# Optimization experiments

Hardware: AMD Instinct MI355X
Metric: run time of the kernel (lower is better)

Reference implementation:

```python
import jax, jax.numpy as jnp
import numpy as np
import math

HEAD_DIM = 128
DEPTH = 12
LAMBDA_INIT = 0.8 - 0.6 * math.exp(-0.3 * DEPTH)
EPS = 1e-5
SCALE = 1.0 / math.sqrt(HEAD_DIM / 2)


def setup_inputs() -> dict:
    key = jax.random.key(0)
    ks = jax.random.split(key, 8)
    b, t, d = 2, 4096, 2048
    return {
        "x": jax.random.normal(ks[0], (b, t, d), dtype=jnp.float32),
        "wq": jax.random.normal(ks[1], (d, HEAD_DIM), dtype=jnp.float32) * 0.02,
        "wk": jax.random.normal(ks[2], (d, HEAD_DIM), dtype=jnp.float32) * 0.02,
        "wv": jax.random.normal(ks[3], (d, HEAD_DIM), dtype=jnp.float32) * 0.02,
        "lambda_q1": jax.random.normal(ks[4], (HEAD_DIM // 2,), dtype=jnp.float32) * 0.1,
        "lambda_q2": jax.random.normal(ks[5], (HEAD_DIM // 2,), dtype=jnp.float32) * 0.1,
        "lambda_k1": jax.random.normal(ks[6], (HEAD_DIM // 2,), dtype=jnp.float32) * 0.1,
        "lambda_k2": jax.random.normal(ks[7], (HEAD_DIM // 2,), dtype=jnp.float32) * 0.1,
        "ln_weight": jnp.ones((HEAD_DIM,), dtype=jnp.float32),
    }


def reference(x, wq, wk, wv, lambda_q1, lambda_q2, lambda_k1, lambda_k2, ln_weight):
    b, t, d = x.shape
    q = x @ wq  # [b,t,hd]
    k = x @ wk
    v = x @ wv
    h = HEAD_DIM // 2
    q1, q2 = q[..., :h], q[..., h:]
    k1, k2 = k[..., :h], k[..., h:]
    # causal mask: True where attention is disallowed (strictly upper triangle)
    causal = jnp.triu(jnp.ones((t, t), dtype=bool), k=1)
    neg_inf = jnp.float32(-jnp.inf)

    def masked_softmax(qh, kh):
        scores = jnp.einsum('btd,bsd->bts', qh, kh) * SCALE
        scores = jnp.where(causal, neg_inf, scores)
        return jax.nn.softmax(scores, axis=-1)

    a1 = masked_softmax(q1, k1)
    a2 = masked_softmax(q2, k2)
    lmbda = (jnp.exp(jnp.sum(lambda_q1 * lambda_k1))
             - jnp.exp(jnp.sum(lambda_q2 * lambda_k2))
             + LAMBDA_INIT)
    diffattn = jnp.einsum('bts,bsd->btd', a1 - lmbda * a2, v)
    rms = jnp.sqrt(jnp.mean(diffattn * diffattn, axis=-1, keepdims=True) + EPS)
    out = (1.0 - LAMBDA_INIT) * (diffattn / rms * ln_weight)
    return out
```

## Files before the change

kernel.cpp:

```cpp
#include <hip/hip_runtime.h>
#include <stdint.h>

#define T_SEQ 4096
#define NB 2
#define D_MODEL 2048
#define HD 128

typedef __attribute__((ext_vector_type(4)))  float f32x4;
typedef __attribute__((ext_vector_type(16))) float f32x16;
typedef __attribute__((ext_vector_type(8)))  short bf16x8;
typedef __attribute__((ext_vector_type(4)))  unsigned u32x4;

#define LAMBDA_INIT 0.7836057665316244f
#define OUT_SCALE   0.21639423346837556f

__device__ __forceinline__ unsigned short f2bf(float f) {
  unsigned int u = __float_as_uint(f);
  u += 0x7FFFu + ((u >> 16) & 1u);
  return (unsigned short)(u >> 16);
}
__device__ __forceinline__ float bf2f(unsigned short h) {
  return __uint_as_float(((unsigned int)h) << 16);
}
__device__ __forceinline__ unsigned cvt_pk_bf16(float a, float b) {
  unsigned r;
  asm("v_cvt_pk_bf16_f32 %0, %1, %2" : "=v"(r) : "v"(a), "v"(b));
  return r;
}
__device__ __forceinline__ void gload16(const void* g, void* l) {
  __builtin_amdgcn_global_load_lds(
      (const __attribute__((address_space(1))) unsigned int*)g,
      (__attribute__((address_space(3))) unsigned int*)l, 16, 0, 0);
}

__global__ __launch_bounds__(256) void wtrans(
    const float* __restrict__ wq, const float* __restrict__ wk,
    const float* __restrict__ wv, unsigned short* __restrict__ wT)
{
  const int which = blockIdx.y;
  const int s = blockIdx.x;
  const float* w = (which == 0) ? wq : ((which == 1) ? wk : wv);
  const float scale = (which == 0) ? 0.125f : 1.0f;
  const int tid = threadIdx.x;
  #pragma unroll
  for (int j = 0; j < 4; ++j) {
    int cell = j * 256 + tid;
    int q = cell >> 7, n = cell & 127;
    int kb = s * 64 + q * 8;
    float v[8];
    #pragma unroll
    for (int e = 0; e < 8; ++e) v[e] = w[(size_t)(kb + e) * HD + n] * scale;
    u32x4 pk = { cvt_pk_bf16(v[0], v[1]), cvt_pk_bf16(v[2], v[3]),
                 cvt_pk_bf16(v[4], v[5]), cvt_pk_bf16(v[6], v[7]) };
    *reinterpret_cast<u32x4*>(&wT[(size_t)(which * 32 + s) * 8192 + (size_t)cell * 8]) = pk;
  }
}

__global__ __launch_bounds__(256, 2) void qkv_part(
    const float* __restrict__ x, const unsigned short* __restrict__ wT,
    float* __restrict__ P)
{
  __shared__ __align__(16) char lds[4][16384];
  const int tid = threadIdx.x, lane = tid & 63, wid = tid >> 6;
  const int bid = blockIdx.x;
  const int ks   = bid & 1;
  const int type = (bid >> 1) % 3;
  const int mt   = bid / 6;
  const int wm = wid >> 1, wn = wid & 1;
  const int fr = lane & 15, fq = lane >> 4;
  const int m0 = mt * 64;

  const float* xbase = x + (size_t)m0 * D_MODEL + ks * 1024;
  const unsigned short* wslab = wT + (size_t)type * 262144 + (size_t)(ks * 16) * 8192;

  f32x4 acc[2][4];
  #pragma unroll
  for (int i = 0; i < 2; ++i)
    #pragma unroll
    for (int j = 0; j < 4; ++j) acc[i][j] = (f32x4){0.f, 0.f, 0.f, 0.f};

#define DMA(t) do {                                                        \
    char* As_ = &lds[(t) & 3][0];                                          \
    char* Bs_ = &lds[(t) & 3][8192];                                       \
    const int k0_ = (t) * 32;                                              \
    _Pragma("unroll")                                                      \
    for (int j = 0; j < 2; ++j) {                                          \
      int c = (wid * 2 + j) * 64 + lane;                                   \
      int row = c >> 3, kcp = c & 7;                                       \
      gload16(xbase + (size_t)row * D_MODEL + k0_ + ((kcp ^ (row & 7)) << 2), \
              As_ + (wid * 2 + j) * 1024);                                 \
    }                                                                      \
    const unsigned short* bsrc_ = wslab + (size_t)(t) * 4096;              \
    _Pragma("unroll")                                                      \
    for (int j = 0; j < 2; ++j) {                                          \
      int cb = (wid * 2 + j) * 64;                                         \
      gload16(bsrc_ + (size_t)(cb + lane) * 8, Bs_ + cb * 16);             \
    }                                                                      \
  } while (0)

#define STEP(t, VMIMM) do {                                                \
    asm volatile("s_waitcnt vmcnt(" VMIMM ")" ::: "memory");               \
    __builtin_amdgcn_s_barrier();                                          \
    __builtin_amdgcn_sched_barrier(0);                                     \
    if ((t) + 3 < 32) DMA((t) + 3);                                        \
    __builtin_amdgcn_sched_barrier(0);                                     \
    const char* Ac_ = &lds[(t) & 3][0];                                    \
    const char* Bc_ = &lds[(t) & 3][8192];                                 \
    bf16x8 af_[2];                                                         \
    _Pragma("unroll")                                                      \
    for (int mi = 0; mi < 2; ++mi) {                                       \
      int row = wm * 32 + mi * 16 + fr;                                    \
      int p1 = (2 * fq) ^ (row & 7), p2 = (2 * fq + 1) ^ (row & 7);        \
      f32x4 lo = *reinterpret_cast<const f32x4*>(Ac_ + (row * 8 + p1) * 16); \
      f32x4 hi = *reinterpret_cast<const f32x4*>(Ac_ + (row * 8 + p2) * 16); \
      u32x4 pk = { cvt_pk_bf16(lo[0], lo[1]), cvt_pk_bf16(lo[2], lo[3]),   \
                   cvt_pk_bf16(hi[0], hi[1]), cvt_pk_bf16(hi[2], hi[3]) }; \
      af_[mi] = *reinterpret_cast<bf16x8*>(&pk);                           \
    }                                                                      \
    _Pragma("unroll")                                                      \
    for (int ni = 0; ni < 4; ++ni) {                                       \
      int n = wn * 64 + ni * 16 + fr;                                      \
      bf16x8 bf_ = *reinterpret_cast<const bf16x8*>(Bc_ + (fq * 128 + n) * 16); \
      acc[0][ni] = __builtin_amdgcn_mfma_f32_16x16x32_bf16(af_[0], bf_, acc[0][ni], 0, 0, 0); \
      acc[1][ni] = __builtin_amdgcn_mfma_f32_16x16x32_bf16(af_[1], bf_, acc[1][ni], 0, 0, 0); \
    }                                                                      \
  } while (0)

  DMA(0); DMA(1); DMA(2);
  #pragma unroll 1
  for (int t = 0; t < 30; ++t) STEP(t, "8");
  STEP(30, "4");
  STEP(31, "0");
#undef STEP
#undef DMA

  float* pp = P + ((size_t)(ks * 3 + type) * 8192 + m0) * 128;
  #pragma unroll
  for (int mi = 0; mi < 2; ++mi)
    #pragma unroll
    for (int ni = 0; ni < 4; ++ni)
      #pragma unroll
      for (int r = 0; r < 4; ++r)
        pp[(size_t)(wm * 32 + mi * 16 + fq * 4 + r) * 128 + wn * 64 + ni * 16 + fr]
            = acc[mi][ni][r];
}

__global__ __launch_bounds__(256) void qkv_merge(
    const float* __restrict__ P,
    unsigned short* __restrict__ qb, unsigned short* __restrict__ kS,
    unsigned short* __restrict__ vS)
{
  const int gid = blockIdx.x * 256 + threadIdx.x;
  const size_t e8 = (size_t)gid * 8;
  const int type = (int)(e8 >> 20);
  const int rem  = (int)(e8 & 1048575);
  const int m = rem >> 7, n0 = rem & 127;
  const float* p0 = P + (size_t)type * 1048576 + rem;
  const float* p1 = p0 + (size_t)3 * 1048576;
  f32x4 a0 = *reinterpret_cast<const f32x4*>(p0);
  f32x4 a1 = *reinterpret_cast<const f32x4*>(p0 + 4);
  f32x4 b0 = *reinterpret_cast<const f32x4*>(p1);
  f32x4 b1 = *reinterpret_cast<const f32x4*>(p1 + 4);
  float s[8];
  #pragma unroll
  for (int j = 0; j < 4; ++j) { s[j] = a0[j] + b0[j]; s[4 + j] = a1[j] + b1[j]; }
  u32x4 pk = { cvt_pk_bf16(s[0], s[1]), cvt_pk_bf16(s[2], s[3]),
               cvt_pk_bf16(s[4], s[5]), cvt_pk_bf16(s[6], s[7]) };

  const int bb = m >> 12, tt = m & 4095;
  const int kt = tt >> 5, kvl = tt & 31;
  if (type == 0) {
    *reinterpret_cast<u32x4*>(&qb[(size_t)m * HD + n0]) = pk;
  } else if (type == 1) {
    int g = n0 >> 6, hl = n0 & 63;
    int ksf = hl >> 4, r8 = (hl >> 3) & 1;
    size_t idx = ((((((size_t)bb * 128 + kt) * 2 + g) * 4) + ksf) << 9)
               + (size_t)(kvl + 32 * r8) * 8;
    *reinterpret_cast<u32x4*>(&kS[idx]) = pk;
  } else {
    int f = kvl >> 4, r8v = (kvl >> 3) & 1, e = kvl & 7;
    #pragma unroll
    for (int j = 0; j < 8; ++j) {
      int n = n0 + j;
      int vcb = n >> 5;
      size_t idx = (((((size_t)bb * 128 + kt) * 8) + vcb * 2 + f) << 9)
                 + (size_t)((n & 31) + 32 * r8v) * 8 + e;
      vS[idx] = f2bf(s[j]);
    }
  }
}

template<int LOG2S>
__global__ __launch_bounds__(256, 2) void diff_attn_part(
    const unsigned short* __restrict__ qb, const unsigned short* __restrict__ kS,
    const unsigned short* __restrict__ vS,
    unsigned short* __restrict__ po, float* __restrict__ pm, float* __restrict__ pl)
{
  constexpr int S = 1 << LOG2S;
  const int tid = threadIdx.x, lane = tid & 63, wid = tid >> 6;
  const int wave_id = blockIdx.x * 4 + wid;
  const int sp = wave_id & (S - 1);
  const int g  = (wave_id >> LOG2S) & 1;
  const int qt_raw = (wave_id >> (LOG2S + 1)) & 127;
  const int b  = wave_id >> (LOG2S + 8);
  const int qt = 127 - qt_raw;
  const int slot = (((b * 128 + qt) * 2 + g) << LOG2S) + sp;
  const int lq = lane & 31, lh = lane >> 5;
  const int q0 = qt * 32;
  const int n  = qt + 1;
  const int kt0 = (n * sp) >> LOG2S;
  const int kt1 = (n * (sp + 1)) >> LOG2S;

  bf16x8 qf[4];
  const unsigned short* qp = qb + ((size_t)b * T_SEQ + q0 + lq) * HD + g * 64 + lh * 8;
  #pragma unroll
  for (int ks = 0; ks < 4; ++ks) qf[ks] = *reinterpret_cast<const bf16x8*>(qp + ks * 16);

  f32x16 acc[4];
  #pragma unroll
  for (int v = 0; v < 4; ++v)
    #pragma unroll
    for (int r = 0; r < 16; ++r) acc[v][r] = 0.f;
  float mrun = -1e30f, lrun = 0.f;

  const unsigned short* kbase = kS + ((size_t)(b * 128) * 2 + g) * 4 * 512 + lane * 8;
  const unsigned short* vbase = vS + (size_t)(b * 128) * 8 * 512 + lane * 8;
  #define KFRAG(kt, ks) (kbase + ((size_t)(kt) * 8 + (ks)) * 512)
  #define VFRAG(kt, f)  (vbase + ((size_t)(kt) * 8 + (f)) * 512)

  bf16x8 kf[4];
  if (kt0 < kt1) {
    #pragma unroll
    for (int ks = 0; ks < 4; ++ks)
      kf[ks] = *reinterpret_cast<const bf16x8*>(KFRAG(kt0, ks));
  }

  for (int kt = kt0; kt < kt1; ++kt) {
    bf16x8 vfa[4], vfb[4];
    #pragma unroll
    for (int vcb = 0; vcb < 4; ++vcb) {
      vfa[vcb] = *reinterpret_cast<const bf16x8*>(VFRAG(kt, vcb * 2));
      vfb[vcb] = *reinterpret_cast<const bf16x8*>(VFRAG(kt, vcb * 2 + 1));
    }
    bf16x8 kfn[4];
    const bool more = (kt + 1 < kt1);
    if (more) {
      #pragma unroll
      for (int ks = 0; ks < 4; ++ks)
        kfn[ks] = *reinterpret_cast<const bf16x8*>(KFRAG(kt + 1, ks));
    }
    f32x16 sc;
    #pragma unroll
    for (int r = 0; r < 16; ++r) sc[r] = 0.f;
    #pragma unroll
    for (int ks = 0; ks < 4; ++ks)
      sc = __builtin_amdgcn_mfma_f32_32x32x16_bf16(kf[ks], qf[ks], sc, 0, 0, 0);

    float p[16];
    if (kt == n - 1) {
      #pragma unroll
      for (int r = 0; r < 16; ++r) {
        int rloc = (r & 3) + 8 * (r >> 2) + 4 * lh;
        p[r] = (rloc > lq) ? -1e30f : sc[r];
      }
    } else {
      #pragma unroll
      for (int r = 0; r < 16; ++r) p[r] = sc[r];
    }
    float t16[16];
    #pragma unroll
    for (int r = 0; r < 16; ++r) t16[r] = p[r];
    #pragma unroll
    for (int st = 8; st >= 1; st >>= 1)
      #pragma unroll
      for (int r = 0; r < 8; ++r)
        if (r < st) t16[r] = fmaxf(t16[r], t16[r + st]);
    float pmax = fmaxf(t16[0], __shfl_xor(t16[0], 32));
    if (__any(pmax > mrun + 8.f)) {
      float mn = fmaxf(mrun, pmax);
      float al = __expf(mrun - mn);
      lrun *= al;
      #pragma unroll
      for (int v = 0; v < 4; ++v)
        #pragma unroll
        for (int r = 0; r < 16; ++r) acc[v][r] *= al;
      mrun = mn;
    }
    float psum;
    {
      float s16[16];
      #pragma unroll
      for (int r = 0; r < 16; ++r) { p[r] = __expf(p[r] - mrun); s16[r] = p[r]; }
      #pragma unroll
      for (int st = 8; st >= 1; st >>= 1)
        #pragma unroll
        for (int r = 0; r < 8; ++r)
          if (r < st) s16[r] += s16[r + st];
      psum = s16[0];
    }
    lrun += psum + __shfl_xor(psum, 32);

    unsigned A0 = cvt_pk_bf16(p[0],  p[1]),  A1 = cvt_pk_bf16(p[2],  p[3]);
    unsigned A2 = cvt_pk_bf16(p[4],  p[5]),  A3 = cvt_pk_bf16(p[6],  p[7]);
    unsigned A4 = cvt_pk_bf16(p[8],  p[9]),  A5 = cvt_pk_bf16(p[10], p[11]);
    unsigned A6 = cvt_pk_bf16(p[12], p[13]), A7 = cvt_pk_bf16(p[14], p[15]);
    unsigned pA0 = (unsigned)__shfl_xor((int)A0, 32);
    unsigned pA1 = (unsigned)__shfl_xor((int)A1, 32);
    unsigned pA2 = (unsigned)__shfl_xor((int)A2, 32);
    unsigned pA3 = (unsigned)__shfl_xor((int)A3, 32);
    unsigned pA4 = (unsigned)__shfl_xor((int)A4, 32);
    unsigned pA5 = (unsigned)__shfl_xor((int)A5, 32);
    unsigned pA6 = (unsigned)__shfl_xor((int)A6, 32);
    unsigned pA7 = (unsigned)__shfl_xor((int)A7, 32);
    u32x4 w0, w1;
    w0[0] = lh ? pA2 : A0;  w0[1] = lh ? pA3 : A1;
    w0[2] = lh ? A2  : pA0; w0[3] = lh ? A3  : pA1;
    w1[0] = lh ? pA6 : A4;  w1[1] = lh ? pA7 : A5;
    w1[2] = lh ? A6  : pA4; w1[3] = lh ? A7  : pA5;
    bf16x8 pb0 = *reinterpret_cast<bf16x8*>(&w0);
    bf16x8 pb1 = *reinterpret_cast<bf16x8*>(&w1);
    #pragma unroll
    for (int vcb = 0; vcb < 4; ++vcb) {
      acc[vcb] = __builtin_amdgcn_mfma_f32_32x32x16_bf16(vfa[vcb], pb0, acc[vcb], 0, 0, 0);
      acc[vcb] = __builtin_amdgcn_mfma_f32_32x32x16_bf16(vfb[vcb], pb1, acc[vcb], 0, 0, 0);
    }
    if (more) {
      #pragma unroll
      for (int ks = 0; ks < 4; ++ks) kf[ks] = kfn[ks];
    }
  }
  #undef KFRAG
  #undef VFRAG
  const size_t pbase = (size_t)slot * (HD * 32);
  #pragma unroll
  for (int vcb = 0; vcb < 4; ++vcb)
    #pragma unroll
    for (int r = 0; r < 16; ++r) {
      int vc = vcb * 32 + (r & 3) + 8 * (r >> 2) + 4 * lh;
      po[pbase + (size_t)vc * 32 + lq] = f2bf(acc[vcb][r]);
    }
  if (lane < 32) {
    pm[slot * 32 + lq] = mrun;
    pl[slot * 32 + lq] = lrun;
  }
}

template<int LOG2S>
__global__ __launch_bounds__(256) void diff_merge(
    const unsigned short* __restrict__ po, const float* __restrict__ pm,
    const float* __restrict__ pl,
    const float* __restrict__ lq1, const float* __restrict__ lq2,
    const float* __restrict__ lk1, const float* __restrict__ lk2,
    const float* __restrict__ lnw, float* __restrict__ out)
{
  constexpr int S = 1 << LOG2S;
  __shared__ float red[4][32];
  const int tid = threadIdx.x, lane = tid & 63, wid = tid >> 6;
  const int q = tid & 31, vg = tid >> 5;
  const int bq = blockIdx.x;
  const int b = bq >> 7, qt = bq & 127;

  float la = lq1[lane] * lk1[lane];
  float lb = lq2[lane] * lk2[lane];
  #pragma unroll
  for (int off = 32; off >= 1; off >>= 1) {
    la += __shfl_xor(la, off);
    lb += __shfl_xor(lb, off);
  }
  const float lam = __expf(la) - __expf(lb) + LAMBDA_INIT;

  const int p1 = (bq * 2 + 0) * S;
  const int p2 = (bq * 2 + 1) * S;
  float w1[S], w2[S];
  {
    float ms[S];
    #pragma unroll
    for (int s = 0; s < S; ++s) ms[s] = pm[(p1 + s) * 32 + q];
    float M = ms[0];
    #pragma unroll
    for (int s = 1; s < S; ++s) M = fmaxf(M, ms[s]);
    float L = 0.f;
    #pragma unroll
    for (int s = 0; s < S; ++s) { w1[s] = __expf(ms[s] - M); L += w1[s] * pl[(p1 + s) * 32 + q]; }
    float inv = 1.f / L;
    #pragma unroll
    for (int s = 0; s < S; ++s) w1[s] *= inv;
  }
  {
    float ms[S];
    #pragma unroll
    for (int s = 0; s < S; ++s) ms[s] = pm[(p2 + s) * 32 + q];
    float M = ms[0];
    #pragma unroll
    for (int s = 1; s < S; ++s) M = fmaxf(M, ms[s]);
    float L = 0.f;
    #pragma unroll
    for (int s = 0; s < S; ++s) { w2[s] = __expf(ms[s] - M); L += w2[s] * pl[(p2 + s) * 32 + q]; }
    float inv = lam / L;
    #pragma unroll
    for (int s = 0; s < S; ++s) w2[s] *= inv;
  }
  float d[16], ss = 0.f;
  #pragma unroll
  for (int i = 0; i < 16; ++i) {
    int vc = vg * 16 + i;
    float a1 = 0.f, a2 = 0.f;
    #pragma unroll
    for (int s = 0; s < S; ++s) {
      a1 += w1[s] * bf2f(po[(size_t)(p1 + s) * (HD * 32) + (size_t)vc * 32 + q]);
      a2 += w2[s] * bf2f(po[(size_t)(p2 + s) * (HD * 32) + (size_t)vc * 32 + q]);
    }
    d[i] = a1 - a2;
    ss += d[i] * d[i];
  }
  ss += __shfl_xor(ss, 32);
  if (lane < 32) red[wid][q] = ss;
  __syncthreads();
  float tot = red[0][q] + red[1][q] + red[2][q] + red[3][q];
  float rinv = 1.f / sqrtf(tot * (1.0f / HD) + 1e-5f);
  float* op = out + ((size_t)b * T_SEQ + qt * 32 + q) * HD + vg * 16;
  #pragma unroll
  for (int i = 0; i < 16; ++i) op[i] = OUT_SCALE * d[i] * rinv * lnw[vg * 16 + i];
}

extern "C" void kernel_launch(void* const* d_in, const int* in_sizes, int n_in,
                              void* d_out, int out_size, void* d_ws, size_t ws_size,
                              hipStream_t stream) {
  const float* x   = (const float*)d_in[0];
  const float* wq  = (const float*)d_in[1];
  const float* wk  = (const float*)d_in[2];
  const float* wv  = (const float*)d_in[3];
  const float* lq1 = (const float*)d_in[4];
  const float* lq2 = (const float*)d_in[5];
  const float* lk1 = (const float*)d_in[6];
  const float* lk2 = (const float*)d_in[7];
  const float* lnw = (const float*)d_in[8];
  float* out = (float*)d_out;

  const size_t N = (size_t)NB * T_SEQ * HD;
  const size_t WTN = (size_t)3 * 32 * 8192;
  const size_t PB  = (size_t)2 * 3 * 8192 * 128 * 4;
  int log2S = 3;
  size_t parts = 0, region = 0;
  for (;; --log2S) {
    parts = ((size_t)NB * 128 * 2) << log2S;
    size_t pob = parts * (HD * 32) * 2;
    size_t rmin = PB + WTN * 2;
    region = (pob > rmin) ? pob : rmin;
    size_t need = 3 * N * 2 + region + parts * 32 * 8;
    if (need <= ws_size || log2S == 0) break;
  }

  unsigned short* qb = (unsigned short*)d_ws;
  unsigned short* kS = qb + N;
  unsigned short* vS = kS + N;
  unsigned short* po = vS + N;
  float* Ppart = (float*)po;
  unsigned short* wT = (unsigned short*)((char*)po + region) - WTN;
  float* pm = (float*)((char*)po + region);
  float* pl = pm + parts * 32;

  wtrans<<<dim3(32, 3), 256, 0, stream>>>(wq, wk, wv, wT);
  qkv_part<<<dim3(768), 256, 0, stream>>>(x, wT, Ppart);
  qkv_merge<<<dim3(1536), 256, 0, stream>>>(Ppart, qb, kS, vS);
  const int ablocks = (int)(parts / 4);
  switch (log2S) {
    case 3:
      diff_attn_part<3><<<dim3(ablocks), 256, 0, stream>>>(qb, kS, vS, po, pm, pl);
      diff_merge<3><<<dim3(NB * 128), 256, 0, stream>>>(po, pm, pl, lq1, lq2, lk1, lk2, lnw, out);
      break;
    case 2:
      diff_attn_part<2><<<dim3(ablocks), 256, 0, stream>>>(qb, kS, vS, po, pm, pl);
      diff_merge<2><<<dim3(NB * 128), 256, 0, stream>>>(po, pm, pl, lq1, lq2, lk1, lk2, lnw, out);
      break;
    case 1:
      diff_attn_part<1><<<dim3(ablocks), 256, 0, stream>>>(qb, kS, vS, po, pm, pl);
      diff_merge<1><<<dim3(NB * 128), 256, 0, stream>>>(po, pm, pl, lq1, lq2, lk1, lk2, lnw, out);
      break;
    default:
      diff_attn_part<0><<<dim3(ablocks), 256, 0, stream>>>(qb, kS, vS, po, pm, pl);
      diff_merge<0><<<dim3(NB * 128), 256, 0, stream>>>(po, pm, pl, lq1, lq2, lk1, lk2, lnw, out);
      break;
  }
}
```

Before: 89.38 us.

## Compute Q, K and V in one block to reuse each x tile

The QKV projection block now computes all three outputs (Q, K, V) for its row tile instead of one, so each x tile is loaded from global memory once rather than three times. LDS per stage grows to hold three weight slices, the grid shrinks to a third, and occupancy drops to one block per CU. The wait counts are adjusted for the larger number of loads per stage. The intent is to cut redundant reads of the large fp32 input, at the cost of less latency hiding and higher register pressure.

```diff
diff --git a/kernel.cpp b/kernel.cpp
--- a/kernel.cpp
+++ b/kernel.cpp
@@ -56,28 +56,29 @@
   }
 }
 
-__global__ __launch_bounds__(256, 2) void qkv_part(
+__global__ __launch_bounds__(256, 1) void qkv_part(
     const float* __restrict__ x, const unsigned short* __restrict__ wT,
     float* __restrict__ P)
 {
-  __shared__ __align__(16) char lds[4][16384];
+  __shared__ __align__(16) char lds[4][32768];
   const int tid = threadIdx.x, lane = tid & 63, wid = tid >> 6;
   const int bid = blockIdx.x;
-  const int ks   = bid & 1;
-  const int type = (bid >> 1) % 3;
-  const int mt   = bid / 6;
+  const int ks = bid & 1;
+  const int mt = bid >> 1;
   const int wm = wid >> 1, wn = wid & 1;
   const int fr = lane & 15, fq = lane >> 4;
   const int m0 = mt * 64;
 
   const float* xbase = x + (size_t)m0 * D_MODEL + ks * 1024;
-  const unsigned short* wslab = wT + (size_t)type * 262144 + (size_t)(ks * 16) * 8192;
-
-  f32x4 acc[2][4];
-  #pragma unroll
-  for (int i = 0; i < 2; ++i)
-    #pragma unroll
-    for (int j = 0; j < 4; ++j) acc[i][j] = (f32x4){0.f, 0.f, 0.f, 0.f};
+  const unsigned short* wbase = wT + (size_t)(ks * 16) * 8192;
+
+  f32x4 acc[3][2][4];
+  #pragma unroll
+  for (int ty = 0; ty < 3; ++ty)
+    #pragma unroll
+    for (int i = 0; i < 2; ++i)
+      #pragma unroll
+      for (int j = 0; j < 4; ++j) acc[ty][i][j] = (f32x4){0.f, 0.f, 0.f, 0.f};
 
 #define DMA(t) do {                                                        \
     char* As_ = &lds[(t) & 3][0];                                          \
@@ -90,11 +91,17 @@
       gload16(xbase + (size_t)row * D_MODEL + k0_ + ((kcp ^ (row & 7)) << 2), \
               As_ + (wid * 2 + j) * 1024);                                 \
     }                                                                      \
-    const unsigned short* bsrc_ = wslab + (size_t)(t) * 4096;              \
     _Pragma("unroll")                                                      \
-    for (int j = 0; j < 2; ++j) {                                          \
-      int cb = (wid * 2 + j) * 64;                                         \
-      gload16(bsrc_ + (size_t)(cb + lane) * 8, Bs_ + cb * 16);             \
+    for (int ty = 0; ty < 3; ++ty) {                                       \
+      const unsigned short* bs_ = wbase + (size_t)ty * 262144              \
+                                + (size_t)((t) >> 1) * 8192                \
+                                + (size_t)((t) & 1) * 4096;                \
+      _Pragma("unroll")                                                    \
+      for (int j = 0; j < 2; ++j) {                                        \
+        int cb = (wid * 2 + j) * 64;                                       \
+        gload16(bs_ + (size_t)(cb + lane) * 8,                             \
+                Bs_ + (size_t)ty * 8192 + cb * 16);                        \
+      }                                                                    \
     }                                                                      \
   } while (0)
 
@@ -118,31 +125,38 @@
       af_[mi] = *reinterpret_cast<bf16x8*>(&pk);                           \
     }                                                                      \
     _Pragma("unroll")                                                      \
-    for (int ni = 0; ni < 4; ++ni) {                                       \
-      int n = wn * 64 + ni * 16 + fr;                                      \
-      bf16x8 bf_ = *reinterpret_cast<const bf16x8*>(Bc_ + (fq * 128 + n) * 16); \
-      acc[0][ni] = __builtin_amdgcn_mfma_f32_16x16x32_bf16(af_[0], bf_, acc[0][ni], 0, 0, 0); \
-      acc[1][ni] = __builtin_amdgcn_mfma_f32_16x16x32_bf16(af_[1], bf_, acc[1][ni], 0, 0, 0); \
-    }                                                                      \
+    for (int ty = 0; ty < 3; ++ty)                                         \
+      _Pragma("unroll")                                                    \
+      for (int ni = 0; ni < 4; ++ni) {                                     \
+        int n = wn * 64 + ni * 16 + fr;                                    \
+        bf16x8 bf_ = *reinterpret_cast<const bf16x8*>(                     \
+            Bc_ + (size_t)ty * 8192 + (fq * 128 + n) * 16);                \
+        acc[ty][0][ni] = __builtin_amdgcn_mfma_f32_16x16x32_bf16(af_[0], bf_, acc[ty][0][ni], 0, 0, 0); \
+        acc[ty][1][ni] = __builtin_amdgcn_mfma_f32_16x16x32_bf16(af_[1], bf_, acc[ty][1][ni], 0, 0, 0); \
+      }                                                                    \
   } while (0)
 
   DMA(0); DMA(1); DMA(2);
   #pragma unroll 1
-  for (int t = 0; t < 30; ++t) STEP(t, "8");
-  STEP(30, "4");
+  for (int t = 0; t < 29; ++t) STEP(t, "16");
+  STEP(29, "16");
+  STEP(30, "8");
   STEP(31, "0");
 #undef STEP
 #undef DMA
 
-  float* pp = P + ((size_t)(ks * 3 + type) * 8192 + m0) * 128;
-  #pragma unroll
-  for (int mi = 0; mi < 2; ++mi)
-    #pragma unroll
-    for (int ni = 0; ni < 4; ++ni)
-      #pragma unroll
-      for (int r = 0; r < 4; ++r)
-        pp[(size_t)(wm * 32 + mi * 16 + fq * 4 + r) * 128 + wn * 64 + ni * 16 + fr]
-            = acc[mi][ni][r];
+  #pragma unroll
+  for (int ty = 0; ty < 3; ++ty) {
+    float* pp = P + ((size_t)(ks * 3 + ty) * 8192 + m0) * 128;
+    #pragma unroll
+    for (int mi = 0; mi < 2; ++mi)
+      #pragma unroll
+      for (int ni = 0; ni < 4; ++ni)
+        #pragma unroll
+        for (int r = 0; r < 4; ++r)
+          pp[(size_t)(wm * 32 + mi * 16 + fq * 4 + r) * 128 + wn * 64 + ni * 16 + fr]
+              = acc[ty][mi][ni][r];
+  }
 }
 
 __global__ __launch_bounds__(256) void qkv_merge(
@@ -461,7 +475,7 @@
   float* pl = pm + parts * 32;
 
   wtrans<<<dim3(32, 3), 256, 0, stream>>>(wq, wk, wv, wT);
-  qkv_part<<<dim3(768), 256, 0, stream>>>(x, wT, Ppart);
+  qkv_part<<<dim3(256), 256, 0, stream>>>(x, wT, Ppart);
   qkv_merge<<<dim3(1536), 256, 0, stream>>>(Ppart, qb, kS, vS);
   const int ablocks = (int)(parts / 4);
   switch (log2S) {
```

New measurement: 79.58 us. -11.0%, faster.
